# Kernel optimization log

Measured on AMD Instinct MI355X. Metric: run time of the kernel, lower is better.

Reference implementation:

```python
import jax, jax.numpy as jnp
import numpy as np

B, T_TRG, T_SRC, C, H = 2, 2048, 2048, 512, 8
HD = C // H

def setup_inputs() -> dict:
    key = jax.random.key(0)
    ks = jax.random.split(key, 10)
    s = 0.02
    return {
        'x': jax.random.normal(ks[0], (B, T_TRG, C), jnp.float32),
        'encoder_outputs': jax.random.normal(ks[1], (B, T_SRC, C), jnp.float32),
        'padding_mask': jnp.ones((B, T_SRC), jnp.int32),
        'Wq': jax.random.normal(ks[2], (C, C), jnp.float32) * s,
        'bq': jnp.zeros((C,), jnp.float32),
        'Wk': jax.random.normal(ks[3], (C, C), jnp.float32) * s,
        'bk': jnp.zeros((C,), jnp.float32),
        'Wv': jax.random.normal(ks[4], (C, C), jnp.float32) * s,
        'bv': jnp.zeros((C,), jnp.float32),
        'Wo': jax.random.normal(ks[5], (C, C), jnp.float32) * s,
        'bo': jnp.zeros((C,), jnp.float32),
    }

def reference(x, encoder_outputs, padding_mask, Wq, bq, Wk, bk, Wv, bv, Wo, bo):
    Bx, Tt, Cx = x.shape
    Ts = encoder_outputs.shape[1]
    scale = HD ** -0.5
    # projections (nn.Linear: y = x @ W.T + b; here W stored as [in,out])
    q = (x @ Wq + bq).reshape(Bx, Tt, H, HD).transpose(0, 2, 1, 3)            # [B,H,Tt,HD]
    k = (encoder_outputs @ Wk + bk).reshape(Bx, Ts, H, HD).transpose(0, 2, 1, 3)
    v = (encoder_outputs @ Wv + bv).reshape(Bx, Ts, H, HD).transpose(0, 2, 1, 3)
    scores = jnp.einsum('bhqd,bhkd->bhqk', q, k) * scale                      # [B,H,Tt,Ts]
    mask = padding_mask[:, None, None, :] != 0                                # [B,1,1,Ts]
    scores = jnp.where(mask, scores, jnp.float32(-jnp.inf))
    probs = jax.nn.softmax(scores, axis=-1)
    # dropout: identity at inference
    out = jnp.einsum('bhqk,bhkd->bhqd', probs, v)                             # [B,H,Tt,HD]
    out = out.transpose(0, 2, 1, 3).reshape(Bx, Tt, Cx)
    return out @ Wo + bo
```

## Files before the change

kernel.cpp:

```cpp
#include <hip/hip_runtime.h>

#define TT 2048
#define TS 2048
#define NB 2
#define CC 512
#define NH 8
#define HD 64
#define NCH 4
#define KCH (TS / NCH)
#define NROW (NB * NH * TT)

typedef __attribute__((ext_vector_type(8))) short s8v;
typedef __attribute__((ext_vector_type(8))) __bf16 bf8v;
typedef __attribute__((ext_vector_type(4))) float f4v;
typedef __attribute__((ext_vector_type(4))) unsigned short us4;

static __device__ __forceinline__ unsigned short f2bf(float f) {
  unsigned int u = __builtin_bit_cast(unsigned int, f);
  u += 0x7FFFu + ((u >> 16) & 1u);
  return (unsigned short)(u >> 16);
}
static __device__ __forceinline__ float bf2f(unsigned short u) {
  return __builtin_bit_cast(float, (unsigned int)u << 16);
}
static __device__ __forceinline__ bf8v ld_bf8(const unsigned short* p) {
  return __builtin_bit_cast(bf8v, *(const s8v*)p);
}
static __device__ __forceinline__ f4v mfma16(bf8v a, bf8v b, f4v c) {
  return __builtin_amdgcn_mfma_f32_16x16x32_bf16(a, b, c, 0, 0, 0);
}
static __device__ __forceinline__ void gll16(const unsigned short* g,
                                             unsigned short* l) {
  __builtin_amdgcn_global_load_lds(
      (const __attribute__((address_space(1))) unsigned int*)g,
      (__attribute__((address_space(3))) unsigned int*)l, 16, 0, 0);
}

__global__ __launch_bounds__(256) void wtrans_k(const float* __restrict__ W0,
    const float* __restrict__ W1, const float* __restrict__ W2, const float* __restrict__ W3,
    unsigned short* __restrict__ T0, unsigned short* __restrict__ T1,
    unsigned short* __restrict__ T2, unsigned short* __restrict__ T3) {
  const float* Ws[4] = {W0, W1, W2, W3};
  unsigned short* Ts[4] = {T0, T1, T2, T3};
  const float* W = Ws[blockIdx.z];
  unsigned short* WT = Ts[blockIdx.z];
  __shared__ float t[64][65];
  int i0 = blockIdx.x * 64, j0 = blockIdx.y * 64;
  int tx = threadIdx.x & 63, ty = threadIdx.x >> 6;
#pragma unroll
  for (int r = 0; r < 16; r++) {
    int li = ty * 16 + r;
    t[li][tx] = W[(size_t)(i0 + li) * CC + j0 + tx];
  }
  __syncthreads();
#pragma unroll
  for (int r = 0; r < 16; r++) {
    int lj = ty * 16 + r;
    WT[(size_t)(j0 + lj) * CC + i0 + tx] = f2bf(t[tx][lj]);
  }
}

__global__ __launch_bounds__(256) void cvt_k(const float* __restrict__ x,
    const float* __restrict__ enc, const int* __restrict__ mask,
    unsigned short* __restrict__ xb, unsigned short* __restrict__ eb,
    float* __restrict__ pinf) {
  size_t t = (size_t)blockIdx.x * 256 + threadIdx.x;
  size_t i = t * 4;
  f4v a = *(const f4v*)(x + i);
  f4v b = *(const f4v*)(enc + i);
  us4 pa, pb;
#pragma unroll
  for (int j = 0; j < 4; j++) { pa[j] = f2bf(a[j]); pb[j] = f2bf(b[j]); }
  *(us4*)(xb + i) = pa;
  *(us4*)(eb + i) = pb;
  if (t < NB * TS) pinf[t] = (mask[t] != 0) ? 0.0f : -1e30f;
}

__global__ __launch_bounds__(256) void gemm128_k(
    const unsigned short* __restrict__ xb, const unsigned short* __restrict__ eb,
    const unsigned short* __restrict__ Attb,
    const unsigned short* __restrict__ WqT, const unsigned short* __restrict__ WkT,
    const unsigned short* __restrict__ WvT, const unsigned short* __restrict__ WoT,
    const float* __restrict__ bq, const float* __restrict__ bk,
    const float* __restrict__ bv, const float* __restrict__ bo,
    unsigned short* __restrict__ Qb, unsigned short* __restrict__ Kb,
    unsigned short* __restrict__ VTb, float* __restrict__ outf, int zbase) {
  __shared__ unsigned short Al[2][128 * 64];
  __shared__ unsigned short Bl[2][64 * 64];
  int op = blockIdx.z + zbase;
  const unsigned short* A = (op == 0) ? xb : (op == 3 ? Attb : eb);
  const unsigned short* W = (op == 0) ? WqT : (op == 1 ? WkT : (op == 2 ? WvT : WoT));
  const float* bias = (op == 0) ? bq : (op == 1 ? bk : (op == 2 ? bv : bo));
  int lane = threadIdx.x & 63, wave = threadIdx.x >> 6;
  int quad = lane >> 4, l16 = lane & 15;
  int r8 = lane >> 3, g8 = (lane & 7) ^ r8;
  int m0 = blockIdx.x * 128, n0 = blockIdx.y * 64;
  const unsigned short* Ag = A + (size_t)m0 * CC + g8 * 8;
  const unsigned short* Wg = W + (size_t)n0 * CC + g8 * 8;
  f4v acc[2][4];
#pragma unroll
  for (int s = 0; s < 2; s++)
#pragma unroll
    for (int n = 0; n < 4; n++) acc[s][n] = (f4v){0, 0, 0, 0};
#pragma unroll
  for (int j = 0; j < 4; j++)
    gll16(Ag + (size_t)(wave * 32 + j * 8 + r8) * CC, &Al[0][(wave * 32 + j * 8) * 64]);
#pragma unroll
  for (int j = 0; j < 2; j++)
    gll16(Wg + (size_t)(wave * 16 + j * 8 + r8) * CC, &Bl[0][(wave * 16 + j * 8) * 64]);
  int buf = 0;
  for (int k0 = 0; k0 < CC; k0 += 64) {
    __syncthreads();
    if (k0 + 64 < CC) {
#pragma unroll
      for (int j = 0; j < 4; j++)
        gll16(Ag + (size_t)(wave * 32 + j * 8 + r8) * CC + k0 + 64,
              &Al[buf ^ 1][(wave * 32 + j * 8) * 64]);
#pragma unroll
      for (int j = 0; j < 2; j++)
        gll16(Wg + (size_t)(wave * 16 + j * 8 + r8) * CC + k0 + 64,
              &Bl[buf ^ 1][(wave * 16 + j * 8) * 64]);
    }
    int sw = (quad ^ (l16 & 7)) * 8;
    bf8v af[2][2], bf[4][2];
#pragma unroll
    for (int sub = 0; sub < 2; sub++)
#pragma unroll
      for (int kk = 0; kk < 2; kk++)
        af[sub][kk] = ld_bf8(&Al[buf][(wave * 32 + sub * 16 + l16) * 64 + (sw ^ (kk * 32))]);
#pragma unroll
    for (int nt = 0; nt < 4; nt++)
#pragma unroll
      for (int kk = 0; kk < 2; kk++)
        bf[nt][kk] = ld_bf8(&Bl[buf][(nt * 16 + l16) * 64 + (sw ^ (kk * 32))]);
#pragma unroll
    for (int kk = 0; kk < 2; kk++)
#pragma unroll
      for (int sub = 0; sub < 2; sub++)
#pragma unroll
        for (int nt = 0; nt < 4; nt++)
          acc[sub][nt] = mfma16(af[sub][kk], bf[nt][kk], acc[sub][nt]);
    buf ^= 1;
  }
  const float QSC = 0.125f * 1.44269504088896340736f;
#pragma unroll
  for (int sub = 0; sub < 2; sub++) {
    int row0 = m0 + wave * 32 + sub * 16 + quad * 4;
#pragma unroll
    for (int nt = 0; nt < 4; nt++) {
      int col = n0 + nt * 16 + l16;
      float bcol = bias[col];
      if (op == 3) {
#pragma unroll
        for (int r = 0; r < 4; r++)
          outf[(size_t)(row0 + r) * CC + col] = acc[sub][nt][r] + bcol;
      } else if (op == 2) {
        int bb = row0 >> 11, tt = row0 & (TT - 1);
        us4 pk;
#pragma unroll
        for (int r = 0; r < 4; r++) pk[r] = f2bf(acc[sub][nt][r] + bcol);
        *(us4*)(VTb + ((size_t)bb * CC + col) * TS + tt) = pk;
      } else {
        unsigned short* O = (op == 0) ? Qb : Kb;
        float sc = (op == 0) ? QSC : 1.0f;
#pragma unroll
        for (int r = 0; r < 4; r++)
          O[(size_t)(row0 + r) * CC + col] = f2bf((acc[sub][nt][r] + bcol) * sc);
      }
    }
  }
}

__global__ __launch_bounds__(256) void attn_k(const unsigned short* __restrict__ Q,
    const unsigned short* __restrict__ K, const unsigned short* __restrict__ VT,
    const float* __restrict__ pinf, unsigned short* __restrict__ Op,
    float* __restrict__ Lp) {
  __shared__ unsigned short Kl[2][64 * 64];
  __shared__ unsigned short Vl[2][64 * 64];
  __shared__ unsigned short Pl[4][16][72];
  int lane = threadIdx.x & 63, wave = threadIdx.x >> 6;
  int quad = lane >> 4, l16 = lane & 15;
  int r8 = lane >> 3, g8 = (lane & 7) ^ r8;
  int id = blockIdx.x;
  int bh = id & 15, qblk = (id >> 4) & 15, chunk = id >> 8;
  int b = bh >> 3, h = bh & 7;
  int q0 = qblk * 128 + wave * 32;
  int ck0 = chunk * KCH;

  bf8v qa[2][2];
#pragma unroll
  for (int sub = 0; sub < 2; sub++) {
    const unsigned short* qp =
        Q + (size_t)(b * TT + q0 + sub * 16 + l16) * CC + h * HD + quad * 8;
    qa[sub][0] = ld_bf8(qp);
    qa[sub][1] = ld_bf8(qp + 32);
  }

  f4v o[2][4];
#pragma unroll
  for (int s = 0; s < 2; s++)
#pragma unroll
    for (int d = 0; d < 4; d++) o[s][d] = (f4v){0, 0, 0, 0};
  f4v ls[2] = {{0, 0, 0, 0}, {0, 0, 0, 0}};
  const float* prow = pinf + (size_t)b * TS + ck0;
  const unsigned short* Kg = K + (size_t)(b * TS + ck0) * CC + h * HD + g8 * 8;
  const unsigned short* Vg = VT + ((size_t)b * CC + h * HD) * TS + ck0 + g8 * 8;

#pragma unroll
  for (int j = 0; j < 2; j++) {
    int row = wave * 16 + j * 8;
    gll16(Kg + (size_t)(row + r8) * CC, &Kl[0][row * 64]);
    gll16(Vg + (size_t)(row + r8) * TS, &Vl[0][row * 64]);
  }
  int buf = 0;
  for (int kt = 0; kt < KCH; kt += 64) {
    __syncthreads();
    if (kt + 64 < KCH) {
#pragma unroll
      for (int j = 0; j < 2; j++) {
        int row = wave * 16 + j * 8;
        gll16(Kg + (size_t)(kt + 64 + row + r8) * CC, &Kl[buf ^ 1][row * 64]);
        gll16(Vg + (size_t)(row + r8) * TS + kt + 64, &Vl[buf ^ 1][row * 64]);
      }
    }
    int sw = (quad ^ (l16 & 7)) * 8;
    bf8v kf[4][2];
#pragma unroll
    for (int nt = 0; nt < 4; nt++) {
      kf[nt][0] = ld_bf8(&Kl[buf][(nt * 16 + l16) * 64 + sw]);
      kf[nt][1] = ld_bf8(&Kl[buf][(nt * 16 + l16) * 64 + (sw ^ 32)]);
    }
#pragma unroll
    for (int sub = 0; sub < 2; sub++) {
      f4v s[4];
#pragma unroll
      for (int nt = 0; nt < 4; nt++) {
        f4v z = *(const f4v*)(prow + kt + nt * 16 + quad * 4);
        z = mfma16(kf[nt][0], qa[sub][0], z);
        z = mfma16(kf[nt][1], qa[sub][1], z);
        s[nt] = z;
      }
#pragma unroll
      for (int nt = 0; nt < 4; nt++) {
        us4 pk;
#pragma unroll
        for (int r = 0; r < 4; r++) {
          float p = __builtin_amdgcn_exp2f(s[nt][r]);
          s[nt][r] = p;
          pk[r] = f2bf(p);
        }
        ls[sub] += s[nt];
        *(us4*)&Pl[wave][l16][nt * 16 + quad * 4] = pk;
      }
      bf8v pb0 = ld_bf8(&Pl[wave][l16][quad * 8]);
      bf8v pb1 = ld_bf8(&Pl[wave][l16][32 + quad * 8]);
#pragma unroll
      for (int dt = 0; dt < 4; dt++) {
        bf8v v0 = ld_bf8(&Vl[buf][(dt * 16 + l16) * 64 + sw]);
        bf8v v1 = ld_bf8(&Vl[buf][(dt * 16 + l16) * 64 + (sw ^ 32)]);
        o[sub][dt] = mfma16(v0, pb0, o[sub][dt]);
        o[sub][dt] = mfma16(v1, pb1, o[sub][dt]);
      }
    }
    buf ^= 1;
  }
#pragma unroll
  for (int sub = 0; sub < 2; sub++) {
    float l = (ls[sub][0] + ls[sub][1]) + (ls[sub][2] + ls[sub][3]);
    l += __shfl_xor(l, 16, 64);
    l += __shfl_xor(l, 32, 64);
    int rowb = (b * NH + h) * TT + q0 + sub * 16;
    size_t obase = (size_t)chunk * NROW * HD + (size_t)(rowb + l16) * HD;
#pragma unroll
    for (int dt = 0; dt < 4; dt++) {
      us4 pk;
#pragma unroll
      for (int r = 0; r < 4; r++) pk[r] = f2bf(o[sub][dt][r]);
      *(us4*)&Op[obase + dt * 16 + quad * 4] = pk;
    }
    if (quad == 0) Lp[(size_t)chunk * NROW + rowb + l16] = l;
  }
}

__global__ __launch_bounds__(256) void combine_k(const unsigned short* __restrict__ Op,
    const float* __restrict__ Lp, unsigned short* __restrict__ Attb) {
  int row = blockIdx.x * 4 + (threadIdx.x >> 6);
  int d = threadIdx.x & 63;
  float L = 0.f, o = 0.f;
#pragma unroll
  for (int c = 0; c < NCH; c++) {
    L += Lp[(size_t)c * NROW + row];
    o += bf2f(Op[(size_t)c * NROW * HD + (size_t)row * HD + d]);
  }
  int b = row >> 14, h = (row >> 11) & 7, q = row & (TT - 1);
  Attb[((size_t)(b * TT + q)) * CC + h * HD + d] = f2bf(o / L);
}

extern "C" void kernel_launch(void* const* d_in, const int* in_sizes, int n_in,
                              void* d_out, int out_size, void* d_ws, size_t ws_size,
                              hipStream_t stream) {
  const float* x   = (const float*)d_in[0];
  const float* enc = (const float*)d_in[1];
  const int*   msk = (const int*)d_in[2];
  const float* Wq  = (const float*)d_in[3];
  const float* bq  = (const float*)d_in[4];
  const float* Wk  = (const float*)d_in[5];
  const float* bk  = (const float*)d_in[6];
  const float* Wv  = (const float*)d_in[7];
  const float* bv  = (const float*)d_in[8];
  const float* Wo  = (const float*)d_in[9];
  const float* bo  = (const float*)d_in[10];
  float* out = (float*)d_out;

  char* ws = (char*)d_ws;
  const size_t MB = 1024 * 1024;
  unsigned short* WqT  = (unsigned short*)(ws);
  unsigned short* WkT  = (unsigned short*)(ws + 512 * 1024);
  unsigned short* WvT  = (unsigned short*)(ws + 1024 * 1024);
  unsigned short* WoT  = (unsigned short*)(ws + 1536 * 1024);
  unsigned short* Qb   = (unsigned short*)(ws + 2 * MB);
  unsigned short* Kb   = (unsigned short*)(ws + 6 * MB);
  unsigned short* VTb  = (unsigned short*)(ws + 10 * MB);
  unsigned short* Attb = (unsigned short*)(ws + 14 * MB);
  unsigned short* xb   = (unsigned short*)(ws + 18 * MB);
  unsigned short* eb   = (unsigned short*)(ws + 22 * MB);
  unsigned short* Opart = (unsigned short*)(ws + 18 * MB);
  float* Lp   = (float*)(ws + 34 * MB);
  float* pinf = (float*)(ws + 35 * MB);

  dim3 blk(256);
  wtrans_k<<<dim3(8, 8, 4), blk, 0, stream>>>(Wq, Wk, Wv, Wo, WqT, WkT, WvT, WoT);
  cvt_k<<<dim3(2048), blk, 0, stream>>>(x, enc, msk, xb, eb, pinf);

  gemm128_k<<<dim3(32, 8, 3), blk, 0, stream>>>(xb, eb, Attb, WqT, WkT, WvT, WoT,
                                                bq, bk, bv, bo, Qb, Kb, VTb, out, 0);

  attn_k<<<dim3(1024), blk, 0, stream>>>(Qb, Kb, VTb, pinf, Opart, Lp);
  combine_k<<<dim3(NROW / 4), blk, 0, stream>>>(Opart, Lp, Attb);

  gemm128_k<<<dim3(32, 8, 1), blk, 0, stream>>>(xb, eb, Attb, WqT, WkT, WvT, WoT,
                                                bq, bk, bv, bo, Qb, Kb, VTb, out, 3);
}
```

Baseline: 152.2 us.

## Fuse prep kernels and split-K combine into output GEMM, halve key chunks

Merges weight transpose and input conversion into one launch. Folds the split-KV partial combine and normalization into the output projection's A-tile staging, so the separate combine kernel and its intermediate buffer go away. Reduces key chunks from 4 to 2, which halves partial traffic but also halves the attention grid to 512 blocks. Hoists V fragment loads out of the per-sub loop. The trade-off is fewer attention blocks and register-staged (not async) A loads in the output GEMM.

```diff
diff --git a/kernel.cpp b/kernel.cpp
--- a/kernel.cpp
+++ b/kernel.cpp
@@ -6,7 +6,7 @@
 #define CC 512
 #define NH 8
 #define HD 64
-#define NCH 4
+#define NCH 2
 #define KCH (TS / NCH)
 #define NROW (NB * NH * TT)
 
@@ -36,61 +36,62 @@
       (__attribute__((address_space(3))) unsigned int*)l, 16, 0, 0);
 }
 
-__global__ __launch_bounds__(256) void wtrans_k(const float* __restrict__ W0,
+__global__ __launch_bounds__(256) void prep_k(const float* __restrict__ W0,
     const float* __restrict__ W1, const float* __restrict__ W2, const float* __restrict__ W3,
     unsigned short* __restrict__ T0, unsigned short* __restrict__ T1,
-    unsigned short* __restrict__ T2, unsigned short* __restrict__ T3) {
-  const float* Ws[4] = {W0, W1, W2, W3};
-  unsigned short* Ts[4] = {T0, T1, T2, T3};
-  const float* W = Ws[blockIdx.z];
-  unsigned short* WT = Ts[blockIdx.z];
+    unsigned short* __restrict__ T2, unsigned short* __restrict__ T3,
+    const float* __restrict__ x, const float* __restrict__ enc,
+    const int* __restrict__ mask, unsigned short* __restrict__ xb,
+    unsigned short* __restrict__ eb, float* __restrict__ pinf) {
   __shared__ float t[64][65];
-  int i0 = blockIdx.x * 64, j0 = blockIdx.y * 64;
-  int tx = threadIdx.x & 63, ty = threadIdx.x >> 6;
-#pragma unroll
-  for (int r = 0; r < 16; r++) {
-    int li = ty * 16 + r;
-    t[li][tx] = W[(size_t)(i0 + li) * CC + j0 + tx];
-  }
-  __syncthreads();
-#pragma unroll
-  for (int r = 0; r < 16; r++) {
-    int lj = ty * 16 + r;
-    WT[(size_t)(j0 + lj) * CC + i0 + tx] = f2bf(t[tx][lj]);
-  }
-}
-
-__global__ __launch_bounds__(256) void cvt_k(const float* __restrict__ x,
-    const float* __restrict__ enc, const int* __restrict__ mask,
-    unsigned short* __restrict__ xb, unsigned short* __restrict__ eb,
-    float* __restrict__ pinf) {
-  size_t t = (size_t)blockIdx.x * 256 + threadIdx.x;
-  size_t i = t * 4;
-  f4v a = *(const f4v*)(x + i);
-  f4v b = *(const f4v*)(enc + i);
-  us4 pa, pb;
-#pragma unroll
-  for (int j = 0; j < 4; j++) { pa[j] = f2bf(a[j]); pb[j] = f2bf(b[j]); }
-  *(us4*)(xb + i) = pa;
-  *(us4*)(eb + i) = pb;
-  if (t < NB * TS) pinf[t] = (mask[t] != 0) ? 0.0f : -1e30f;
-}
-
-__global__ __launch_bounds__(256) void gemm128_k(
+  int id = blockIdx.x;
+  if (id < 256) {
+    const float* Ws[4] = {W0, W1, W2, W3};
+    unsigned short* Ts[4] = {T0, T1, T2, T3};
+    const float* W = Ws[id >> 6];
+    unsigned short* WT = Ts[id >> 6];
+    int blk = id & 63;
+    int i0 = (blk >> 3) * 64, j0 = (blk & 7) * 64;
+    int tx = threadIdx.x & 63, ty = threadIdx.x >> 6;
+#pragma unroll
+    for (int r = 0; r < 16; r++) {
+      int li = ty * 16 + r;
+      t[li][tx] = W[(size_t)(i0 + li) * CC + j0 + tx];
+    }
+    __syncthreads();
+#pragma unroll
+    for (int r = 0; r < 16; r++) {
+      int lj = ty * 16 + r;
+      WT[(size_t)(j0 + lj) * CC + i0 + tx] = f2bf(t[tx][lj]);
+    }
+  } else {
+    size_t tt = (size_t)(id - 256) * 256 + threadIdx.x;
+    size_t i = tt * 4;
+    f4v a = *(const f4v*)(x + i);
+    f4v b = *(const f4v*)(enc + i);
+    us4 pa, pb;
+#pragma unroll
+    for (int j = 0; j < 4; j++) { pa[j] = f2bf(a[j]); pb[j] = f2bf(b[j]); }
+    *(us4*)(xb + i) = pa;
+    *(us4*)(eb + i) = pb;
+    if (tt < NB * TS) pinf[tt] = (mask[tt] != 0) ? 0.0f : -1e30f;
+  }
+}
+
+__global__ __launch_bounds__(256) void qkv_k(
     const unsigned short* __restrict__ xb, const unsigned short* __restrict__ eb,
-    const unsigned short* __restrict__ Attb,
     const unsigned short* __restrict__ WqT, const unsigned short* __restrict__ WkT,
-    const unsigned short* __restrict__ WvT, const unsigned short* __restrict__ WoT,
+    const unsigned short* __restrict__ WvT,
     const float* __restrict__ bq, const float* __restrict__ bk,
-    const float* __restrict__ bv, const float* __restrict__ bo,
+    const float* __restrict__ bv,
     unsigned short* __restrict__ Qb, unsigned short* __restrict__ Kb,
-    unsigned short* __restrict__ VTb, float* __restrict__ outf, int zbase) {
+    unsigned short* __restrict__ VTb) {
   __shared__ unsigned short Al[2][128 * 64];
   __shared__ unsigned short Bl[2][64 * 64];
-  int op = blockIdx.z + zbase;
-  const unsigned short* A = (op == 0) ? xb : (op == 3 ? Attb : eb);
-  const unsigned short* W = (op == 0) ? WqT : (op == 1 ? WkT : (op == 2 ? WvT : WoT));
-  const float* bias = (op == 0) ? bq : (op == 1 ? bk : (op == 2 ? bv : bo));
+  int op = blockIdx.z;
+  const unsigned short* A = (op == 0) ? xb : eb;
+  const unsigned short* W = (op == 0) ? WqT : (op == 1 ? WkT : WvT);
+  const float* bias = (op == 0) ? bq : (op == 1 ? bk : bv);
   int lane = threadIdx.x & 63, wave = threadIdx.x >> 6;
   int quad = lane >> 4, l16 = lane & 15;
   int r8 = lane >> 3, g8 = (lane & 7) ^ r8;
@@ -122,7 +123,7 @@
               &Bl[buf ^ 1][(wave * 16 + j * 8) * 64]);
     }
     int sw = (quad ^ (l16 & 7)) * 8;
-    bf8v af[2][2], bf[4][2];
+    bf8v af[2][2], bfr[4][2];
 #pragma unroll
     for (int sub = 0; sub < 2; sub++)
 #pragma unroll
@@ -132,14 +133,14 @@
     for (int nt = 0; nt < 4; nt++)
 #pragma unroll
       for (int kk = 0; kk < 2; kk++)
-        bf[nt][kk] = ld_bf8(&Bl[buf][(nt * 16 + l16) * 64 + (sw ^ (kk * 32))]);
+        bfr[nt][kk] = ld_bf8(&Bl[buf][(nt * 16 + l16) * 64 + (sw ^ (kk * 32))]);
 #pragma unroll
     for (int kk = 0; kk < 2; kk++)
 #pragma unroll
       for (int sub = 0; sub < 2; sub++)
 #pragma unroll
         for (int nt = 0; nt < 4; nt++)
-          acc[sub][nt] = mfma16(af[sub][kk], bf[nt][kk], acc[sub][nt]);
+          acc[sub][nt] = mfma16(af[sub][kk], bfr[nt][kk], acc[sub][nt]);
     buf ^= 1;
   }
   const float QSC = 0.125f * 1.44269504088896340736f;
@@ -150,11 +151,7 @@
     for (int nt = 0; nt < 4; nt++) {
       int col = n0 + nt * 16 + l16;
       float bcol = bias[col];
-      if (op == 3) {
-#pragma unroll
-        for (int r = 0; r < 4; r++)
-          outf[(size_t)(row0 + r) * CC + col] = acc[sub][nt][r] + bcol;
-      } else if (op == 2) {
+      if (op == 2) {
         int bb = row0 >> 11, tt = row0 & (TT - 1);
         us4 pk;
 #pragma unroll
@@ -177,7 +174,7 @@
     float* __restrict__ Lp) {
   __shared__ unsigned short Kl[2][64 * 64];
   __shared__ unsigned short Vl[2][64 * 64];
-  __shared__ unsigned short Pl[4][16][72];
+  __shared__ unsigned short Pl[4][2][16 * 72];
   int lane = threadIdx.x & 63, wave = threadIdx.x >> 6;
   int quad = lane >> 4, l16 = lane & 15;
   int r8 = lane >> 3, g8 = (lane & 7) ^ r8;
@@ -224,11 +221,13 @@
       }
     }
     int sw = (quad ^ (l16 & 7)) * 8;
-    bf8v kf[4][2];
+    bf8v kf[4][2], vf[4][2];
 #pragma unroll
     for (int nt = 0; nt < 4; nt++) {
       kf[nt][0] = ld_bf8(&Kl[buf][(nt * 16 + l16) * 64 + sw]);
       kf[nt][1] = ld_bf8(&Kl[buf][(nt * 16 + l16) * 64 + (sw ^ 32)]);
+      vf[nt][0] = ld_bf8(&Vl[buf][(nt * 16 + l16) * 64 + sw]);
+      vf[nt][1] = ld_bf8(&Vl[buf][(nt * 16 + l16) * 64 + (sw ^ 32)]);
     }
 #pragma unroll
     for (int sub = 0; sub < 2; sub++) {
@@ -240,6 +239,7 @@
         z = mfma16(kf[nt][1], qa[sub][1], z);
         s[nt] = z;
       }
+      unsigned short* pw = &Pl[wave][sub][0];
 #pragma unroll
       for (int nt = 0; nt < 4; nt++) {
         us4 pk;
@@ -250,16 +250,14 @@
           pk[r] = f2bf(p);
         }
         ls[sub] += s[nt];
-        *(us4*)&Pl[wave][l16][nt * 16 + quad * 4] = pk;
-      }
-      bf8v pb0 = ld_bf8(&Pl[wave][l16][quad * 8]);
-      bf8v pb1 = ld_bf8(&Pl[wave][l16][32 + quad * 8]);
+        *(us4*)&pw[l16 * 72 + nt * 16 + quad * 4] = pk;
+      }
+      bf8v pb0 = ld_bf8(&pw[l16 * 72 + quad * 8]);
+      bf8v pb1 = ld_bf8(&pw[l16 * 72 + 32 + quad * 8]);
 #pragma unroll
       for (int dt = 0; dt < 4; dt++) {
-        bf8v v0 = ld_bf8(&Vl[buf][(dt * 16 + l16) * 64 + sw]);
-        bf8v v1 = ld_bf8(&Vl[buf][(dt * 16 + l16) * 64 + (sw ^ 32)]);
-        o[sub][dt] = mfma16(v0, pb0, o[sub][dt]);
-        o[sub][dt] = mfma16(v1, pb1, o[sub][dt]);
+        o[sub][dt] = mfma16(vf[dt][0], pb0, o[sub][dt]);
+        o[sub][dt] = mfma16(vf[dt][1], pb1, o[sub][dt]);
       }
     }
     buf ^= 1;
@@ -282,18 +280,92 @@
   }
 }
 
-__global__ __launch_bounds__(256) void combine_k(const unsigned short* __restrict__ Op,
-    const float* __restrict__ Lp, unsigned short* __restrict__ Attb) {
-  int row = blockIdx.x * 4 + (threadIdx.x >> 6);
-  int d = threadIdx.x & 63;
-  float L = 0.f, o = 0.f;
-#pragma unroll
-  for (int c = 0; c < NCH; c++) {
-    L += Lp[(size_t)c * NROW + row];
-    o += bf2f(Op[(size_t)c * NROW * HD + (size_t)row * HD + d]);
-  }
-  int b = row >> 14, h = (row >> 11) & 7, q = row & (TT - 1);
-  Attb[((size_t)(b * TT + q)) * CC + h * HD + d] = f2bf(o / L);
+__global__ __launch_bounds__(256) void gemmo_k(const unsigned short* __restrict__ Op,
+    const float* __restrict__ Lp, const unsigned short* __restrict__ WoT,
+    const float* __restrict__ bo, float* __restrict__ outf) {
+  __shared__ unsigned short Al[2][128 * 64];
+  __shared__ unsigned short Bl[2][64 * 64];
+  int lane = threadIdx.x & 63, wave = threadIdx.x >> 6;
+  int quad = lane >> 4, l16 = lane & 15;
+  int r8 = lane >> 3, lc = lane & 7, g8 = lc ^ r8;
+  int m0 = blockIdx.x * 128, n0 = blockIdx.y * 64;
+  const unsigned short* Wg = WoT + (size_t)n0 * CC + g8 * 8;
+  f4v acc[2][4];
+#pragma unroll
+  for (int s = 0; s < 2; s++)
+#pragma unroll
+    for (int n = 0; n < 4; n++) acc[s][n] = (f4v){0, 0, 0, 0};
+
+  auto stage_a = [&](int k0, int dbuf) {
+    int h = k0 >> 6;
+#pragma unroll
+    for (int j = 0; j < 4; j++) {
+      int rr = wave * 32 + j * 8 + r8;
+      int m = m0 + rr;
+      int bb = m >> 11, q = m & (TT - 1);
+      size_t rowb = (size_t)((bb * NH + h) * TT + q);
+      int gd = (lc ^ r8) * 8;
+      s8v o0 = *(const s8v*)(Op + rowb * HD + gd);
+      s8v o1 = *(const s8v*)(Op + (size_t)NROW * HD + rowb * HD + gd);
+      float L = Lp[rowb] + Lp[NROW + rowb];
+      float inv = __builtin_amdgcn_rcpf(L);
+      s8v pk;
+#pragma unroll
+      for (int e = 0; e < 8; e++) {
+        float v = (bf2f((unsigned short)o0[e]) + bf2f((unsigned short)o1[e])) * inv;
+        pk[e] = (short)f2bf(v);
+      }
+      *(s8v*)&Al[dbuf][rr * 64 + lc * 8] = pk;
+    }
+  };
+
+  stage_a(0, 0);
+#pragma unroll
+  for (int j = 0; j < 2; j++)
+    gll16(Wg + (size_t)(wave * 16 + j * 8 + r8) * CC, &Bl[0][(wave * 16 + j * 8) * 64]);
+  int buf = 0;
+  for (int k0 = 0; k0 < CC; k0 += 64) {
+    __syncthreads();
+    if (k0 + 64 < CC) {
+      stage_a(k0 + 64, buf ^ 1);
+#pragma unroll
+      for (int j = 0; j < 2; j++)
+        gll16(Wg + (size_t)(wave * 16 + j * 8 + r8) * CC + k0 + 64,
+              &Bl[buf ^ 1][(wave * 16 + j * 8) * 64]);
+    }
+    int sw = (quad ^ (l16 & 7)) * 8;
+    bf8v af[2][2], bfr[4][2];
+#pragma unroll
+    for (int sub = 0; sub < 2; sub++)
+#pragma unroll
+      for (int kk = 0; kk < 2; kk++)
+        af[sub][kk] = ld_bf8(&Al[buf][(wave * 32 + sub * 16 + l16) * 64 + (sw ^ (kk * 32))]);
+#pragma unroll
+    for (int nt = 0; nt < 4; nt++)
+#pragma unroll
+      for (int kk = 0; kk < 2; kk++)
+        bfr[nt][kk] = ld_bf8(&Bl[buf][(nt * 16 + l16) * 64 + (sw ^ (kk * 32))]);
+#pragma unroll
+    for (int kk = 0; kk < 2; kk++)
+#pragma unroll
+      for (int sub = 0; sub < 2; sub++)
+#pragma unroll
+        for (int nt = 0; nt < 4; nt++)
+          acc[sub][nt] = mfma16(af[sub][kk], bfr[nt][kk], acc[sub][nt]);
+    buf ^= 1;
+  }
+#pragma unroll
+  for (int sub = 0; sub < 2; sub++) {
+    int row0 = m0 + wave * 32 + sub * 16 + quad * 4;
+#pragma unroll
+    for (int nt = 0; nt < 4; nt++) {
+      int col = n0 + nt * 16 + l16;
+      float bcol = bo[col];
+#pragma unroll
+      for (int r = 0; r < 4; r++)
+        outf[(size_t)(row0 + r) * CC + col] = acc[sub][nt][r] + bcol;
+    }
+  }
 }
 
 extern "C" void kernel_launch(void* const* d_in, const int* in_sizes, int n_in,
@@ -321,7 +393,6 @@
   unsigned short* Qb   = (unsigned short*)(ws + 2 * MB);
   unsigned short* Kb   = (unsigned short*)(ws + 6 * MB);
   unsigned short* VTb  = (unsigned short*)(ws + 10 * MB);
-  unsigned short* Attb = (unsigned short*)(ws + 14 * MB);
   unsigned short* xb   = (unsigned short*)(ws + 18 * MB);
   unsigned short* eb   = (unsigned short*)(ws + 22 * MB);
   unsigned short* Opart = (unsigned short*)(ws + 18 * MB);
@@ -329,15 +400,13 @@
   float* pinf = (float*)(ws + 35 * MB);
 
   dim3 blk(256);
-  wtrans_k<<<dim3(8, 8, 4), blk, 0, stream>>>(Wq, Wk, Wv, Wo, WqT, WkT, WvT, WoT);
-  cvt_k<<<dim3(2048), blk, 0, stream>>>(x, enc, msk, xb, eb, pinf);
-
-  gemm128_k<<<dim3(32, 8, 3), blk, 0, stream>>>(xb, eb, Attb, WqT, WkT, WvT, WoT,
-                                                bq, bk, bv, bo, Qb, Kb, VTb, out, 0);
-
-  attn_k<<<dim3(1024), blk, 0, stream>>>(Qb, Kb, VTb, pinf, Opart, Lp);
-  combine_k<<<dim3(NROW / 4), blk, 0, stream>>>(Opart, Lp, Attb);
-
-  gemm128_k<<<dim3(32, 8, 1), blk, 0, stream>>>(xb, eb, Attb, WqT, WkT, WvT, WoT,
-                                                bq, bk, bv, bo, Qb, Kb, VTb, out, 3);
-}
+  prep_k<<<dim3(2304), blk, 0, stream>>>(Wq, Wk, Wv, Wo, WqT, WkT, WvT, WoT,
+                                         x, enc, msk, xb, eb, pinf);
+
+  qkv_k<<<dim3(32, 8, 3), blk, 0, stream>>>(xb, eb, WqT, WkT, WvT,
+                                            bq, bk, bv, Qb, Kb, VTb);
+
+  attn_k<<<dim3(512), blk, 0, stream>>>(Qb, Kb, VTb, pinf, Opart, Lp);
+
+  gemmo_k<<<dim3(32, 8), blk, 0, stream>>>(Opart, Lp, WoT, bo, out);
+}
```

Measured after the change: 145.2 us, median of 2. 4.6% less time.
